# Optimization experiments

Hardware: AMD Instinct MI355X
Metric: run time of the kernel (lower is better)

Reference implementation:

```python
import jax, jax.numpy as jnp
import numpy as np

N_WORD, N_TOPIC, N_DOC = 50000, 2000, 50000
D_WORD, D_TOPIC, D_OUT = 256, 128, 128
E_WW, E_WT, E_WD, E_TD, E_TT = 500000, 400000, 500000, 400000, 300000


def setup_inputs() -> dict:
    key = jax.random.key(0)
    ks = jax.random.split(key, 32)
    i = iter(range(32))

    def randn(shape, scale=1.0):
        return jax.random.normal(ks[next(i)], shape, dtype=jnp.float32) * scale

    def edges(n_e, n_src, n_dst):
        src = jax.random.randint(ks[next(i)], (n_e,), 0, n_src, dtype=jnp.int32)
        dst = jax.random.randint(ks[next(i)], (n_e,), 0, n_dst, dtype=jnp.int32)
        w = jax.random.uniform(ks[next(i)], (n_e,), dtype=jnp.float32)
        return src, dst, w

    feat_word = randn((N_WORD, D_WORD))
    feat_topic = randn((N_TOPIC, D_TOPIC))
    ww_src, ww_dst, ww_w = edges(E_WW, N_WORD, N_WORD)
    wt_src, wt_dst, wt_w = edges(E_WT, N_WORD, N_TOPIC)
    wd_src, wd_dst, wd_w = edges(E_WD, N_WORD, N_DOC)
    td_src, td_dst, td_w = edges(E_TD, N_TOPIC, N_DOC)
    tt_src, tt_dst, tt_w = edges(E_TT, N_TOPIC, N_TOPIC)
    return dict(
        feat_word=feat_word, feat_topic=feat_topic,
        ww_src=ww_src, ww_dst=ww_dst, ww_w=ww_w,
        wt_src=wt_src, wt_dst=wt_dst, wt_w=wt_w,
        wd_src=wd_src, wd_dst=wd_dst, wd_w=wd_w,
        td_src=td_src, td_dst=td_dst, td_w=td_w,
        tt_src=tt_src, tt_dst=tt_dst, tt_w=tt_w,
        W_ww=randn((D_WORD, D_OUT), 0.02), b_ww=randn((D_OUT,), 0.02),
        W_wt=randn((D_WORD, D_OUT), 0.02), b_wt=randn((D_OUT,), 0.02),
        W_wd=randn((D_WORD, D_OUT), 0.02), b_wd=randn((D_OUT,), 0.02),
        W_td=randn((D_TOPIC, D_OUT), 0.02), b_td=randn((D_OUT,), 0.02),
        W_tt=randn((D_TOPIC, D_OUT), 0.02), b_tt=randn((D_OUT,), 0.02),
    )


def _mean_agg(Wh, src, dst, w, n_dst):
    # u_mul_e: gather src feature, scale by edge weight; fn.mean: divide by in-degree
    m = Wh[src] * w[:, None]                                   # [E, D_OUT]
    s = jax.ops.segment_sum(m, dst, num_segments=n_dst)        # [n_dst, D_OUT]
    deg = jax.ops.segment_sum(jnp.ones_like(w), dst, num_segments=n_dst)
    return jnp.where(deg[:, None] > 0, s / jnp.maximum(deg, 1.0)[:, None], 0.0)


def reference(feat_word, feat_topic,
              ww_src, ww_dst, ww_w, wt_src, wt_dst, wt_w,
              wd_src, wd_dst, wd_w, td_src, td_dst, td_w,
              tt_src, tt_dst, tt_w,
              W_ww, b_ww, W_wt, b_wt, W_wd, b_wd, W_td, b_td, W_tt, b_tt):
    # Per-relation projections (note: in the torch source the causal/noise
    # branches are overwritten by the plain Linear, so this is the effective math).
    Wh_ww = feat_word @ W_ww + b_ww
    Wh_wt = feat_word @ W_wt + b_wt
    Wh_wd = feat_word @ W_wd + b_wd
    Wh_td = feat_topic @ W_td + b_td
    Wh_tt = feat_topic @ W_tt + b_tt
    # mean per edge type, then cross-etype 'sum' per destination node type
    h_word = _mean_agg(Wh_ww, ww_src, ww_dst, ww_w, N_WORD)
    h_topic = (_mean_agg(Wh_wt, wt_src, wt_dst, wt_w, N_TOPIC)
               + _mean_agg(Wh_tt, tt_src, tt_dst, tt_w, N_TOPIC))
    h_doc = (_mean_agg(Wh_wd, wd_src, wd_dst, wd_w, N_DOC)
             + _mean_agg(Wh_td, td_src, td_dst, td_w, N_DOC))
    return h_word, h_topic, h_doc
```

## Files before the change

### kernel.cpp

```cpp
#include <hip/hip_runtime.h>

typedef short short8 __attribute__((ext_vector_type(8)));
typedef float floatx4 __attribute__((ext_vector_type(4)));

__device__ __forceinline__ float b2f(unsigned int u16) {
    union { unsigned int i; float f; } v;
    v.i = u16 << 16;
    return v.f;
}
__device__ __forceinline__ unsigned short f2b(float f) {
    unsigned int i = __float_as_uint(f);
    unsigned int r = (i + 0x7FFFu + ((i >> 16) & 1u)) >> 16;
    return (unsigned short)r;
}

#define N_WORD  50000
#define N_TOPIC 2000
#define N_DOC   50000
#define CHAIN_END   0xFFFFFFFFu
#define PAY_INVALID 0xFFFFFFFFu
#define NB_GEMM 814
#define NSLOT_WW (N_WORD * 4)
#define NSLOT_WT (N_TOPIC * 4)
#define NSLOT_TT (N_TOPIC * 4)
#define NSLOT_WD (N_DOC * 4)
#define NSLOT_TD (N_DOC * 4)
#define NSLOT_ALL (NSLOT_WW + NSLOT_WT + NSLOT_TT + NSLOT_WD + NSLOT_TD)

__global__ void detect_kernel(const unsigned int* __restrict__ feat_u32,
                              unsigned int* __restrict__ flag)
{
    int cnt = 0;
    for (int i = 0; i < 256; ++i) {
        unsigned int u = feat_u32[i];
        int e = (u >> 7) & 0xFF;
        if (e >= 110 && e <= 140) ++cnt;
    }
    *flag = (cnt > 128) ? 1u : 0u;
}

__global__ __launch_bounds__(256) void swizzle_kernel(
    const void* __restrict__ W0, const void* __restrict__ W1,
    const void* __restrict__ W2, const void* __restrict__ W3,
    const void* __restrict__ W4,
    const void* __restrict__ b0, const void* __restrict__ b1,
    const void* __restrict__ b2, const void* __restrict__ b3,
    const void* __restrict__ b4,
    short8* __restrict__ D0, short8* __restrict__ D1,
    short8* __restrict__ D2, short8* __restrict__ D3,
    short8* __restrict__ D4,
    unsigned short* __restrict__ bias_out,
    const unsigned int* __restrict__ flag_p)
{
    const int w = blockIdx.y;
    const void* W; const void* bs; short8* D; int S;
    switch (w) {
        case 0: W = W0; bs = b0; D = D0; S = 8; break;
        case 1: W = W1; bs = b1; D = D1; S = 8; break;
        case 2: W = W2; bs = b2; D = D2; S = 8; break;
        case 3: W = W3; bs = b3; D = D3; S = 4; break;
        default: W = W4; bs = b4; D = D4; S = 4; break;
    }
    const int n_entries = S * 8 * 64;
    const int mode = (int)*flag_p;
    for (int e = blockIdx.x * 256 + threadIdx.x; e < n_entries; e += 8 * 256) {
        const int lane = e & 63, t = (e >> 6) & 7, s = e >> 9;
        const int q = lane >> 4, n = t * 16 + (lane & 15);
        short8 val;
#pragma unroll
        for (int j = 0; j < 8; ++j) {
            const int k = s * 32 + q * 8 + j;
            unsigned short hv = mode ? ((const unsigned short*)W)[k * 128 + n]
                                     : f2b(((const float*)W)[k * 128 + n]);
            val[j] = (short)hv;
        }
        D[e] = val;
    }
    if (blockIdx.x == 0 && threadIdx.x < 128) {
        bias_out[w * 128 + threadIdx.x] =
            mode ? ((const unsigned short*)bs)[threadIdx.x]
                 : f2b(((const float*)bs)[threadIdx.x]);
    }
}

template <int S, int NP>
__device__ __forceinline__ void gemm_body_lds(
    short8* __restrict__ Blds,
    const void* feat_, int n_rows, int bx,
    const short8* Ba, const short8* Bb, const short8* Bc,
    const unsigned short* bias_all, int ba, int bb, int bc,
    unsigned short* Oa, unsigned short* Ob, unsigned short* Oc,
    int mode_bf16)
{
    const int tid = threadIdx.x;
    const int lane = tid & 63;
    const int wave = tid >> 6;
    const int row0 = (bx * 4 + wave) * 16;
    const int m = lane & 15, q = lane >> 4;
    const int K = S * 32;
    int arow_idx = row0 + m;
    if (arow_idx >= n_rows) arow_idx = n_rows - 1;

    short8 a[S];
    if (mode_bf16) {
        const short8* arow = (const short8*)((const unsigned short*)feat_ + (size_t)arow_idx * K);
#pragma unroll
        for (int s = 0; s < S; ++s) a[s] = arow[s * 4 + q];
    } else {
        const float* arow = (const float*)feat_ + (size_t)arow_idx * K;
#pragma unroll
        for (int s = 0; s < S; ++s) {
            const float4 f0 = ((const float4*)arow)[s * 8 + q * 2];
            const float4 f1 = ((const float4*)arow)[s * 8 + q * 2 + 1];
            short8 t;
            t[0] = (short)f2b(f0.x); t[1] = (short)f2b(f0.y);
            t[2] = (short)f2b(f0.z); t[3] = (short)f2b(f0.w);
            t[4] = (short)f2b(f1.x); t[5] = (short)f2b(f1.y);
            t[6] = (short)f2b(f1.z); t[7] = (short)f2b(f1.w);
            a[s] = t;
        }
    }

    constexpr int NH = (S * 8 * 64 > 2048) ? 2 : 1;
    constexpr int SH = S / NH;

#pragma unroll
    for (int p = 0; p < NP; ++p) {
        const short8* B = (p == 0) ? Ba : ((p == 1) ? Bb : Bc);
        const unsigned short* bias = bias_all + ((p == 0) ? ba : ((p == 1) ? bb : bc)) * 128;
        unsigned short* O = (p == 0) ? Oa : ((p == 1) ? Ob : Oc);

        floatx4 acc[8];
#pragma unroll
        for (int t = 0; t < 8; ++t) { acc[t][0] = 0.f; acc[t][1] = 0.f; acc[t][2] = 0.f; acc[t][3] = 0.f; }

#pragma unroll
        for (int h = 0; h < NH; ++h) {
            __syncthreads();
            for (int i = tid; i < SH * 8 * 64; i += 256) Blds[i] = B[h * (SH * 8 * 64) + i];
            __syncthreads();
#pragma unroll
            for (int s = 0; s < SH; ++s) {
#pragma unroll
                for (int t = 0; t < 8; ++t) {
                    short8 b = Blds[(s * 8 + t) * 64 + lane];
                    acc[t] = __builtin_amdgcn_mfma_f32_16x16x32_bf16(a[h * SH + s], b, acc[t], 0, 0, 0);
                }
            }
        }

#pragma unroll
        for (int t = 0; t < 8; ++t) {
            const float bb_ = b2f((unsigned int)bias[t * 16 + m]);
#pragma unroll
            for (int r = 0; r < 4; ++r) {
                const int row = row0 + q * 4 + r;
                if (row < n_rows)
                    O[(size_t)row * 128 + t * 16 + m] = f2b(acc[t][r] + bb_);
            }
        }
    }
}

__global__ __launch_bounds__(256) void link_gemm_kernel(
    const void* __restrict__ feat_word, const void* __restrict__ feat_topic,
    const short8* __restrict__ Bww, const short8* __restrict__ Bwt,
    const short8* __restrict__ Bwd, const short8* __restrict__ Btt,
    const short8* __restrict__ Btd,
    const unsigned short* __restrict__ bias_all,
    unsigned short* __restrict__ Wh_ww, unsigned short* __restrict__ Wh_wt,
    unsigned short* __restrict__ Wh_wd, unsigned short* __restrict__ Wh_tt,
    unsigned short* __restrict__ Wh_td,
    const int* s0, const int* d0, const void* w0, int n0, unsigned long long* h0, unsigned long long* e0,
    const int* s1, const int* d1, const void* w1, int n1, unsigned long long* h1, unsigned long long* e1,
    const int* s2, const int* d2, const void* w2, int n2, unsigned long long* h2, unsigned long long* e2,
    const int* s3, const int* d3, const void* w3, int n3, unsigned long long* h3, unsigned long long* e3,
    const int* s4, const int* d4, const void* w4, int n4, unsigned long long* h4, unsigned long long* e4,
    const unsigned int* __restrict__ flag_p)
{
    __shared__ short8 Blds[2048];
    const int mode = (int)*flag_p;

    if (blockIdx.x < NB_GEMM) {
        if (blockIdx.x < 782) {
            gemm_body_lds<8, 3>(Blds, feat_word, N_WORD, blockIdx.x, Bww, Bwt, Bwd,
                                bias_all, 0, 1, 2, Wh_ww, Wh_wt, Wh_wd, mode);
        } else {
            gemm_body_lds<4, 2>(Blds, feat_topic, N_TOPIC, blockIdx.x - 782, Btt, Btd,
                                (const short8*)nullptr, bias_all, 4, 3, 0,
                                Wh_tt, Wh_td, (unsigned short*)nullptr, mode);
        }
        return;
    }

    int lb = blockIdx.x - NB_GEMM;
    const int nb0 = (n0 + 255) >> 8, nb1 = (n1 + 255) >> 8, nb2 = (n2 + 255) >> 8,
              nb3 = (n3 + 255) >> 8;
    const int* src; const int* dst; const void* w_; int n;
    unsigned long long* head8; unsigned long long* ent;
    if (lb < nb0)      { src = s0; dst = d0; w_ = w0; n = n0; head8 = h0; ent = e0; }
    else if ((lb -= nb0) < nb1) { src = s1; dst = d1; w_ = w1; n = n1; head8 = h1; ent = e1; }
    else if ((lb -= nb1) < nb2) { src = s2; dst = d2; w_ = w2; n = n2; head8 = h2; ent = e2; }
    else if ((lb -= nb2) < nb3) { src = s3; dst = d3; w_ = w3; n = n3; head8 = h3; ent = e3; }
    else { lb -= nb3;  src = s4; dst = d4; w_ = w4; n = n4; head8 = h4; ent = e4; }

    const int i = lb * 256 + threadIdx.x;
    if (i >= n) return;
    const int d = dst[i];
    const unsigned short w16 = mode ? ((const unsigned short*)w_)[i]
                                    : f2b(((const float*)w_)[i]);
    const unsigned int pay = ((unsigned int)w16 << 16) | (unsigned int)src[i];
    const unsigned long long X = ((unsigned long long)(unsigned int)i << 32)
                               | (unsigned long long)pay;
    const unsigned int slot = (unsigned int)d * 4 + ((unsigned int)i & 3);
    const unsigned long long old8 = atomicExch(&head8[slot], X);
    ent[i] = old8;
}

__device__ __forceinline__ void acc8(float a[8], const uint4& u, float w)
{
    a[0] += b2f(u.x & 0xffffu) * w; a[1] += b2f(u.x >> 16) * w;
    a[2] += b2f(u.y & 0xffffu) * w; a[3] += b2f(u.y >> 16) * w;
    a[4] += b2f(u.z & 0xffffu) * w; a[5] += b2f(u.z >> 16) * w;
    a[6] += b2f(u.w & 0xffffu) * w; a[7] += b2f(u.w >> 16) * w;
}
__device__ __forceinline__ uint4 rowld(const unsigned short* Wh, unsigned int pay, int sl)
{
    return ((const uint4*)(Wh + (size_t)(pay & 0xffffu) * 128))[sl];
}

__device__ __forceinline__ void walk1e(
    const unsigned long long* __restrict__ ent, const unsigned short* __restrict__ Wh,
    unsigned long long v, int sl, float a[8], float& cnt)
{
    while (true) {
        const unsigned int nx = (unsigned int)(v >> 32);
        const bool ln = (nx != CHAIN_END);
        unsigned long long vn = 0;
        if (ln) vn = ent[nx];
        const unsigned int pay = (unsigned int)v;
        if (pay != PAY_INVALID) {
            const uint4 u = rowld(Wh, pay, sl);
            acc8(a, u, b2f(pay >> 16));
            cnt += 1.0f;
        }
        if (!ln) break;
        v = vn;
    }
}

__device__ __forceinline__ void walk2e(
    const unsigned long long* __restrict__ ent1, const unsigned short* __restrict__ Wh1,
    unsigned long long v1,
    const unsigned long long* __restrict__ ent2, const unsigned short* __restrict__ Wh2,
    unsigned long long v2,
    int sl, float a1[8], float a2[8], float& c1, float& c2)
{
    bool l1 = true, l2 = true;
    while (l1 || l2) {
        const unsigned int n1 = (unsigned int)(v1 >> 32);
        const unsigned int n2 = (unsigned int)(v2 >> 32);
        const bool l1n = l1 && (n1 != CHAIN_END);
        const bool l2n = l2 && (n2 != CHAIN_END);
        unsigned long long v1n = 0, v2n = 0;
        if (l1n) v1n = ent1[n1];
        if (l2n) v2n = ent2[n2];
        const unsigned int p1 = (unsigned int)v1;
        const unsigned int p2 = (unsigned int)v2;
        const bool d1 = l1 && (p1 != PAY_INVALID);
        const bool d2 = l2 && (p2 != PAY_INVALID);
        uint4 u1, u2;
        if (d1) u1 = rowld(Wh1, p1, sl);
        if (d2) u2 = rowld(Wh2, p2, sl);
        if (d1) { acc8(a1, u1, b2f(p1 >> 16)); c1 += 1.0f; }
        if (d2) { acc8(a2, u2, b2f(p2 >> 16)); c2 += 1.0f; }
        v1 = v1n; v2 = v2n; l1 = l1n; l2 = l2n;
    }
}

__device__ __forceinline__ void write8(
    void* out, size_t off_elems, int node, int sl, const float r[8], int mode)
{
    if (mode) {
        uint4 o;
        o.x = (unsigned int)f2b(r[0]) | ((unsigned int)f2b(r[1]) << 16);
        o.y = (unsigned int)f2b(r[2]) | ((unsigned int)f2b(r[3]) << 16);
        o.z = (unsigned int)f2b(r[4]) | ((unsigned int)f2b(r[5]) << 16);
        o.w = (unsigned int)f2b(r[6]) | ((unsigned int)f2b(r[7]) << 16);
        *(uint4*)((unsigned short*)out + off_elems + (size_t)node * 128 + sl * 8) = o;
    } else {
        float* p = (float*)out + off_elems + (size_t)node * 128 + sl * 8;
        ((float4*)p)[0] = make_float4(r[0], r[1], r[2], r[3]);
        ((float4*)p)[1] = make_float4(r[4], r[5], r[6], r[7]);
    }
}

__device__ __forceinline__ void dual_body(
    const unsigned long long* __restrict__ h1, const unsigned long long* __restrict__ e1t,
    const unsigned short* __restrict__ Wh1,
    const unsigned long long* __restrict__ h2, const unsigned long long* __restrict__ e2t,
    const unsigned short* __restrict__ Wh2,
    void* __restrict__ out, size_t off_elems, int blk, int mode)
{
    const int sl = threadIdx.x & 15;
    const int grp = (threadIdx.x >> 4) & 3;
    const int wave = threadIdx.x >> 6;
    const int node = blk * 4 + wave;
    float a1[8] = {0,0,0,0,0,0,0,0}, a2[8] = {0,0,0,0,0,0,0,0};
    float c1 = 0.f, c2 = 0.f;
    walk2e(e1t, Wh1, h1[node * 4 + grp], e2t, Wh2, h2[node * 4 + grp],
           sl, a1, a2, c1, c2);
#pragma unroll
    for (int j = 0; j < 8; ++j) {
        a1[j] += __shfl_xor(a1[j], 16); a1[j] += __shfl_xor(a1[j], 32);
        a2[j] += __shfl_xor(a2[j], 16); a2[j] += __shfl_xor(a2[j], 32);
    }
    c1 += __shfl_xor(c1, 16); c1 += __shfl_xor(c1, 32);
    c2 += __shfl_xor(c2, 16); c2 += __shfl_xor(c2, 32);
    const float i1 = (c1 > 0.f) ? 1.f / c1 : 0.f;
    const float i2 = (c2 > 0.f) ? 1.f / c2 : 0.f;
    float r[8];
#pragma unroll
    for (int j = 0; j < 8; ++j) r[j] = a1[j] * i1 + a2[j] * i2;
    if (grp == 0) write8(out, off_elems, node, sl, r, mode);
}

__global__ __launch_bounds__(256) void gather_dt_kernel(
    const unsigned long long* __restrict__ h_wt, const unsigned long long* __restrict__ e_wt,
    const unsigned short* __restrict__ Wh_wt,
    const unsigned long long* __restrict__ h_tt, const unsigned long long* __restrict__ e_tt,
    const unsigned short* __restrict__ Wh_tt,
    const unsigned long long* __restrict__ h_wd, const unsigned long long* __restrict__ e_wd,
    const unsigned short* __restrict__ Wh_wd,
    const unsigned long long* __restrict__ h_td, const unsigned long long* __restrict__ e_td,
    const unsigned short* __restrict__ Wh_td,
    void* __restrict__ out,
    const unsigned int* __restrict__ flag_p)
{
    const int mode = (int)*flag_p;
    if (blockIdx.x < 500) {
        dual_body(h_wt, e_wt, Wh_wt, h_tt, e_tt, Wh_tt,
                  out, (size_t)6400000, blockIdx.x, mode);
    } else {
        dual_body(h_wd, e_wd, Wh_wd, h_td, e_td, Wh_td,
                  out, (size_t)6656000, blockIdx.x - 500, mode);
    }
}

__global__ __launch_bounds__(256) void gather_w_kernel(
    const unsigned long long* __restrict__ h_ww, const unsigned long long* __restrict__ e_ww,
    const unsigned short* __restrict__ Wh_ww,
    void* __restrict__ out,
    const unsigned int* __restrict__ flag_p)
{
    const int mode = (int)*flag_p;
    const int sl = threadIdx.x & 15;
    const int grp = (threadIdx.x >> 4) & 3;
    const int wave = threadIdx.x >> 6;
    const int node = blockIdx.x * 4 + wave;
    float a[8] = {0,0,0,0,0,0,0,0}; float cnt = 0.f;
    walk1e(e_ww, Wh_ww, h_ww[node * 4 + grp], sl, a, cnt);
#pragma unroll
    for (int j = 0; j < 8; ++j) { a[j] += __shfl_xor(a[j], 16); a[j] += __shfl_xor(a[j], 32); }
    cnt += __shfl_xor(cnt, 16); cnt += __shfl_xor(cnt, 32);
    const float inv = (cnt > 0.f) ? 1.f / cnt : 0.f;
    float r[8];
#pragma unroll
    for (int j = 0; j < 8; ++j) r[j] = a[j] * inv;
    if (grp == 0) write8(out, 0, node, sl, r, mode);
}

extern "C" void kernel_launch(void* const* d_in, const int* in_sizes, int n_in,
                              void* d_out, int out_size, void* d_ws, size_t ws_size,
                              hipStream_t stream)
{
    const void* feat_word  = d_in[0];
    const void* feat_topic = d_in[1];
    const int* ww_src = (const int*)d_in[2];
    const int* ww_dst = (const int*)d_in[3];
    const void* ww_w = d_in[4];
    const int* wt_src = (const int*)d_in[5];
    const int* wt_dst = (const int*)d_in[6];
    const void* wt_w = d_in[7];
    const int* wd_src = (const int*)d_in[8];
    const int* wd_dst = (const int*)d_in[9];
    const void* wd_w = d_in[10];
    const int* td_src = (const int*)d_in[11];
    const int* td_dst = (const int*)d_in[12];
    const void* td_w = d_in[13];
    const int* tt_src = (const int*)d_in[14];
    const int* tt_dst = (const int*)d_in[15];
    const void* tt_w = d_in[16];
    const void* W_ww = d_in[17];
    const void* b_ww = d_in[18];
    const void* W_wt = d_in[19];
    const void* b_wt = d_in[20];
    const void* W_wd = d_in[21];
    const void* b_wd = d_in[22];
    const void* W_td = d_in[23];
    const void* b_td = d_in[24];
    const void* W_tt = d_in[25];
    const void* b_tt = d_in[26];

    const int E_ww = in_sizes[2];
    const int E_wt = in_sizes[5];
    const int E_wd = in_sizes[8];
    const int E_td = in_sizes[11];
    const int E_tt = in_sizes[14];

    char* ws = (char*)d_ws;
    unsigned int* flag = (unsigned int*)ws;
    size_t off = 16;
    unsigned long long* h_ww = (unsigned long long*)(ws + off);
    unsigned long long* h_wt = h_ww + NSLOT_WW;
    unsigned long long* h_tt = h_wt + NSLOT_WT;
    unsigned long long* h_wd = h_tt + NSLOT_TT;
    unsigned long long* h_td = h_wd + NSLOT_WD;
    off += (size_t)NSLOT_ALL * 8;
    off = (off + 15) & ~(size_t)15;
    short8* Bsw_ww = (short8*)(ws + off); off += 65536;
    short8* Bsw_wt = (short8*)(ws + off); off += 65536;
    short8* Bsw_wd = (short8*)(ws + off); off += 65536;
    short8* Bsw_td = (short8*)(ws + off); off += 32768;
    short8* Bsw_tt = (short8*)(ws + off); off += 32768;
    unsigned short* bias_all = (unsigned short*)(ws + off); off += 5 * 128 * 2;
    off = (off + 15) & ~(size_t)15;
    unsigned short* Wh_ww = (unsigned short*)(ws + off); off += (size_t)N_WORD * 128 * 2;
    unsigned short* Wh_wt = (unsigned short*)(ws + off); off += (size_t)N_WORD * 128 * 2;
    unsigned short* Wh_tt = (unsigned short*)(ws + off); off += (size_t)N_TOPIC * 128 * 2;
    unsigned short* Wh_td = (unsigned short*)(ws + off); off += (size_t)N_TOPIC * 128 * 2;
    off = (off + 7) & ~(size_t)7;
    unsigned long long* e_ww = (unsigned long long*)(ws + off); off += (size_t)E_ww * 8;
    unsigned long long* e_wt = (unsigned long long*)(ws + off); off += (size_t)E_wt * 8;
    unsigned long long* e_tt = (unsigned long long*)(ws + off); off += (size_t)E_tt * 8;
    unsigned long long* e_wd = (unsigned long long*)(ws + off); off += (size_t)E_wd * 8;
    unsigned long long* e_td = (unsigned long long*)(ws + off); off += (size_t)E_td * 8;

    unsigned short* Wh_wd = (unsigned short*)d_out;

    detect_kernel<<<1, 1, 0, stream>>>((const unsigned int*)feat_word, flag);
    hipMemsetAsync(h_ww, 0xFF, (size_t)NSLOT_ALL * 8, stream);

    swizzle_kernel<<<dim3(8, 5), 256, 0, stream>>>(
        W_ww, W_wt, W_wd, W_td, W_tt, b_ww, b_wt, b_wd, b_td, b_tt,
        Bsw_ww, Bsw_wt, Bsw_wd, Bsw_td, Bsw_tt, bias_all, flag);

    const int nb_link = ((E_ww + 255) / 256) + ((E_wt + 255) / 256) +
                        ((E_tt + 255) / 256) + ((E_wd + 255) / 256) +
                        ((E_td + 255) / 256);
    link_gemm_kernel<<<NB_GEMM + nb_link, 256, 0, stream>>>(
        feat_word, feat_topic, Bsw_ww, Bsw_wt, Bsw_wd, Bsw_tt, Bsw_td,
        bias_all, Wh_ww, Wh_wt, Wh_wd, Wh_tt, Wh_td,
        ww_src, ww_dst, ww_w, E_ww, h_ww, e_ww,
        wt_src, wt_dst, wt_w, E_wt, h_wt, e_wt,
        tt_src, tt_dst, tt_w, E_tt, h_tt, e_tt,
        wd_src, wd_dst, wd_w, E_wd, h_wd, e_wd,
        td_src, td_dst, td_w, E_td, h_td, e_td, flag);

    gather_dt_kernel<<<500 + 12500, 256, 0, stream>>>(
        h_wt, e_wt, Wh_wt, h_tt, e_tt, Wh_tt,
        h_wd, e_wd, Wh_wd, h_td, e_td, Wh_td, d_out, flag);

    gather_w_kernel<<<12500, 256, 0, stream>>>(
        h_ww, e_ww, Wh_ww, d_out, flag);
}
```

Baseline: 390.2 us.

## Reschedule edge-linking across kernels to overlap with doc gather

The kernel stages are regrouped. Only the wd/td edge-list linking now runs alongside the GEMM. The ww/wt/tt linking moves into the next kernel, where its blocks are interleaved 3:8 with the doc-node gather blocks, and the topic and word gathers are merged into the final kernel. The goal is to overlap atomic-heavy linking with the memory-bound gather and to shorten the GEMM+link kernel so its tail is smaller. The interleaving adds modulo dispatch logic, and the gather blocks may compete for bandwidth with the link blocks.

Result: no change. 390.8 us (+0.2%).

```diff
diff --git a/kernel.cpp b/kernel.cpp
--- a/kernel.cpp
+++ b/kernel.cpp
@@ -162,49 +162,11 @@
     }
 }
 
-__global__ __launch_bounds__(256) void link_gemm_kernel(
-    const void* __restrict__ feat_word, const void* __restrict__ feat_topic,
-    const short8* __restrict__ Bww, const short8* __restrict__ Bwt,
-    const short8* __restrict__ Bwd, const short8* __restrict__ Btt,
-    const short8* __restrict__ Btd,
-    const unsigned short* __restrict__ bias_all,
-    unsigned short* __restrict__ Wh_ww, unsigned short* __restrict__ Wh_wt,
-    unsigned short* __restrict__ Wh_wd, unsigned short* __restrict__ Wh_tt,
-    unsigned short* __restrict__ Wh_td,
-    const int* s0, const int* d0, const void* w0, int n0, unsigned long long* h0, unsigned long long* e0,
-    const int* s1, const int* d1, const void* w1, int n1, unsigned long long* h1, unsigned long long* e1,
-    const int* s2, const int* d2, const void* w2, int n2, unsigned long long* h2, unsigned long long* e2,
-    const int* s3, const int* d3, const void* w3, int n3, unsigned long long* h3, unsigned long long* e3,
-    const int* s4, const int* d4, const void* w4, int n4, unsigned long long* h4, unsigned long long* e4,
-    const unsigned int* __restrict__ flag_p)
-{
-    __shared__ short8 Blds[2048];
-    const int mode = (int)*flag_p;
-
-    if (blockIdx.x < NB_GEMM) {
-        if (blockIdx.x < 782) {
-            gemm_body_lds<8, 3>(Blds, feat_word, N_WORD, blockIdx.x, Bww, Bwt, Bwd,
-                                bias_all, 0, 1, 2, Wh_ww, Wh_wt, Wh_wd, mode);
-        } else {
-            gemm_body_lds<4, 2>(Blds, feat_topic, N_TOPIC, blockIdx.x - 782, Btt, Btd,
-                                (const short8*)nullptr, bias_all, 4, 3, 0,
-                                Wh_tt, Wh_td, (unsigned short*)nullptr, mode);
-        }
-        return;
-    }
-
-    int lb = blockIdx.x - NB_GEMM;
-    const int nb0 = (n0 + 255) >> 8, nb1 = (n1 + 255) >> 8, nb2 = (n2 + 255) >> 8,
-              nb3 = (n3 + 255) >> 8;
-    const int* src; const int* dst; const void* w_; int n;
-    unsigned long long* head8; unsigned long long* ent;
-    if (lb < nb0)      { src = s0; dst = d0; w_ = w0; n = n0; head8 = h0; ent = e0; }
-    else if ((lb -= nb0) < nb1) { src = s1; dst = d1; w_ = w1; n = n1; head8 = h1; ent = e1; }
-    else if ((lb -= nb1) < nb2) { src = s2; dst = d2; w_ = w2; n = n2; head8 = h2; ent = e2; }
-    else if ((lb -= nb2) < nb3) { src = s3; dst = d3; w_ = w3; n = n3; head8 = h3; ent = e3; }
-    else { lb -= nb3;  src = s4; dst = d4; w_ = w4; n = n4; head8 = h4; ent = e4; }
-
-    const int i = lb * 256 + threadIdx.x;
+__device__ __forceinline__ void link_body(
+    const int* __restrict__ src, const int* __restrict__ dst,
+    const void* __restrict__ w_, int n, int i, int mode,
+    unsigned long long* __restrict__ head8, unsigned long long* __restrict__ ent)
+{
     if (i >= n) return;
     const int d = dst[i];
     const unsigned short w16 = mode ? ((const unsigned short*)w_)[i]
@@ -325,11 +287,49 @@
     if (grp == 0) write8(out, off_elems, node, sl, r, mode);
 }
 
-__global__ __launch_bounds__(256) void gather_dt_kernel(
-    const unsigned long long* __restrict__ h_wt, const unsigned long long* __restrict__ e_wt,
-    const unsigned short* __restrict__ Wh_wt,
-    const unsigned long long* __restrict__ h_tt, const unsigned long long* __restrict__ e_tt,
-    const unsigned short* __restrict__ Wh_tt,
+__global__ __launch_bounds__(256) void gemm_linkdt_kernel(
+    const void* __restrict__ feat_word, const void* __restrict__ feat_topic,
+    const short8* __restrict__ Bww, const short8* __restrict__ Bwt,
+    const short8* __restrict__ Bwd, const short8* __restrict__ Btt,
+    const short8* __restrict__ Btd,
+    const unsigned short* __restrict__ bias_all,
+    unsigned short* __restrict__ Wh_ww, unsigned short* __restrict__ Wh_wt,
+    unsigned short* __restrict__ Wh_wd, unsigned short* __restrict__ Wh_tt,
+    unsigned short* __restrict__ Wh_td,
+    const int* s3, const int* d3, const void* w3, int n3,
+    unsigned long long* h3, unsigned long long* e3,
+    const int* s4, const int* d4, const void* w4, int n4,
+    unsigned long long* h4, unsigned long long* e4,
+    const unsigned int* __restrict__ flag_p)
+{
+    __shared__ short8 Blds[2048];
+    const int mode = (int)*flag_p;
+
+    if (blockIdx.x < NB_GEMM) {
+        if (blockIdx.x < 782) {
+            gemm_body_lds<8, 3>(Blds, feat_word, N_WORD, blockIdx.x, Bww, Bwt, Bwd,
+                                bias_all, 0, 1, 2, Wh_ww, Wh_wt, Wh_wd, mode);
+        } else {
+            gemm_body_lds<4, 2>(Blds, feat_topic, N_TOPIC, blockIdx.x - 782, Btt, Btd,
+                                (const short8*)nullptr, bias_all, 4, 3, 0,
+                                Wh_tt, Wh_td, (unsigned short*)nullptr, mode);
+        }
+        return;
+    }
+    int lb = blockIdx.x - NB_GEMM;
+    const int nb3 = (n3 + 255) >> 8;
+    if (lb < nb3) { link_body(s3, d3, w3, n3, lb * 256 + threadIdx.x, mode, h3, e3); return; }
+    lb -= nb3;
+    link_body(s4, d4, w4, n4, lb * 256 + threadIdx.x, mode, h4, e4);
+}
+
+__global__ __launch_bounds__(256) void linkw_gatherdoc_kernel(
+    const int* s0, const int* d0, const void* w0, int n0,
+    unsigned long long* h0, unsigned long long* e0,
+    const int* s1, const int* d1, const void* w1, int n1,
+    unsigned long long* h1, unsigned long long* e1,
+    const int* s2, const int* d2, const void* w2, int n2,
+    unsigned long long* h2, unsigned long long* e2,
     const unsigned long long* __restrict__ h_wd, const unsigned long long* __restrict__ e_wd,
     const unsigned short* __restrict__ Wh_wd,
     const unsigned long long* __restrict__ h_td, const unsigned long long* __restrict__ e_td,
@@ -338,26 +338,43 @@
     const unsigned int* __restrict__ flag_p)
 {
     const int mode = (int)*flag_p;
-    if (blockIdx.x < 500) {
-        dual_body(h_wt, e_wt, Wh_wt, h_tt, e_tt, Wh_tt,
-                  out, (size_t)6400000, blockIdx.x, mode);
-    } else {
-        dual_body(h_wd, e_wd, Wh_wd, h_td, e_td, Wh_td,
-                  out, (size_t)6656000, blockIdx.x - 500, mode);
-    }
-}
-
-__global__ __launch_bounds__(256) void gather_w_kernel(
+    const int per = blockIdx.x / 11, r = blockIdx.x % 11;
+    if (r < 3) {
+        int lid = per * 3 + r;
+        const int nb0 = (n0 + 255) >> 8, nb1 = (n1 + 255) >> 8, nb2 = (n2 + 255) >> 8;
+        if (lid < nb0) { link_body(s0, d0, w0, n0, lid * 256 + threadIdx.x, mode, h0, e0); return; }
+        lid -= nb0;
+        if (lid < nb1) { link_body(s1, d1, w1, n1, lid * 256 + threadIdx.x, mode, h1, e1); return; }
+        lid -= nb1;
+        if (lid < nb2) { link_body(s2, d2, w2, n2, lid * 256 + threadIdx.x, mode, h2, e2); return; }
+        return;
+    }
+    const int did = per * 8 + (r - 3);
+    if (did >= 12500) return;
+    dual_body(h_wd, e_wd, Wh_wd, h_td, e_td, Wh_td,
+              out, (size_t)6656000, did, mode);
+}
+
+__global__ __launch_bounds__(256) void gather_tw_kernel(
+    const unsigned long long* __restrict__ h_wt, const unsigned long long* __restrict__ e_wt,
+    const unsigned short* __restrict__ Wh_wt,
+    const unsigned long long* __restrict__ h_tt, const unsigned long long* __restrict__ e_tt,
+    const unsigned short* __restrict__ Wh_tt,
     const unsigned long long* __restrict__ h_ww, const unsigned long long* __restrict__ e_ww,
     const unsigned short* __restrict__ Wh_ww,
     void* __restrict__ out,
     const unsigned int* __restrict__ flag_p)
 {
     const int mode = (int)*flag_p;
+    if (blockIdx.x < 500) {
+        dual_body(h_wt, e_wt, Wh_wt, h_tt, e_tt, Wh_tt,
+                  out, (size_t)6400000, blockIdx.x, mode);
+        return;
+    }
     const int sl = threadIdx.x & 15;
     const int grp = (threadIdx.x >> 4) & 3;
     const int wave = threadIdx.x >> 6;
-    const int node = blockIdx.x * 4 + wave;
+    const int node = (blockIdx.x - 500) * 4 + wave;
     float a[8] = {0,0,0,0,0,0,0,0}; float cnt = 0.f;
     walk1e(e_ww, Wh_ww, h_ww[node * 4 + grp], sl, a, cnt);
 #pragma unroll
@@ -445,22 +462,26 @@
         W_ww, W_wt, W_wd, W_td, W_tt, b_ww, b_wt, b_wd, b_td, b_tt,
         Bsw_ww, Bsw_wt, Bsw_wd, Bsw_td, Bsw_tt, bias_all, flag);
 
-    const int nb_link = ((E_ww + 255) / 256) + ((E_wt + 255) / 256) +
-                        ((E_tt + 255) / 256) + ((E_wd + 255) / 256) +
-                        ((E_td + 255) / 256);
-    link_gemm_kernel<<<NB_GEMM + nb_link, 256, 0, stream>>>(
+    const int nb_ww = (E_ww + 255) / 256, nb_wt = (E_wt + 255) / 256,
+              nb_tt = (E_tt + 255) / 256, nb_wd = (E_wd + 255) / 256,
+              nb_td = (E_td + 255) / 256;
+
+    gemm_linkdt_kernel<<<NB_GEMM + nb_wd + nb_td, 256, 0, stream>>>(
         feat_word, feat_topic, Bsw_ww, Bsw_wt, Bsw_wd, Bsw_tt, Bsw_td,
         bias_all, Wh_ww, Wh_wt, Wh_wd, Wh_tt, Wh_td,
+        wd_src, wd_dst, wd_w, E_wd, h_wd, e_wd,
+        td_src, td_dst, td_w, E_td, h_td, e_td, flag);
+
+    const int nlink2 = nb_ww + nb_wt + nb_tt;
+    const int per_l = (nlink2 + 2) / 3, per_d = (12500 + 7) / 8;
+    const int periods = (per_l > per_d) ? per_l : per_d;
+    linkw_gatherdoc_kernel<<<periods * 11, 256, 0, stream>>>(
         ww_src, ww_dst, ww_w, E_ww, h_ww, e_ww,
         wt_src, wt_dst, wt_w, E_wt, h_wt, e_wt,
         tt_src, tt_dst, tt_w, E_tt, h_tt, e_tt,
-        wd_src, wd_dst, wd_w, E_wd, h_wd, e_wd,
-        td_src, td_dst, td_w, E_td, h_td, e_td, flag);
-
-    gather_dt_kernel<<<500 + 12500, 256, 0, stream>>>(
+        h_wd, e_wd, Wh_wd, h_td, e_td, Wh_td, d_out, flag);
+
+    gather_tw_kernel<<<500 + 12500, 256, 0, stream>>>(
         h_wt, e_wt, Wh_wt, h_tt, e_tt, Wh_tt,
-        h_wd, e_wd, Wh_wd, h_td, e_td, Wh_td, d_out, flag);
-
-    gather_w_kernel<<<12500, 256, 0, stream>>>(
         h_ww, e_ww, Wh_ww, d_out, flag);
 }
```
